# Kernel tuning notes

Measured on AMD Instinct MI355X. Metric: run time of the kernel, lower is better.

Reference implementation:

```python
import jax, jax.numpy as jnp
import numpy as np

HIDDEN = 4096
N_HEADS = 32
N_KV_HEADS = 8
HEAD_DIM = 128
N_GROUPS = N_HEADS // N_KV_HEADS
ROPE_THETA = 10000.0
QMAX = 127.0
B, S = 1, 2048


def setup_inputs() -> dict:
    key = jax.random.key(0)
    ks = jax.random.split(key, 5)
    hidden_states = jax.random.normal(ks[0], (B, S, HIDDEN), dtype=jnp.float32)
    # additive causal mask (Llama style: 0 on/below diagonal, large negative above)
    tril = jnp.tril(jnp.ones((S, S), dtype=bool))
    attention_mask = jnp.where(tril, 0.0, -1e9).astype(jnp.float32)[None, None]
    position_ids = jnp.arange(S, dtype=jnp.int64 if jax.config.jax_enable_x64 else jnp.int32)[None].astype(jnp.int32)
    sc = 1.0 / np.sqrt(HIDDEN)
    wq = jax.random.normal(ks[1], (HIDDEN, N_HEADS * HEAD_DIM), dtype=jnp.float32) * sc
    wk = jax.random.normal(ks[2], (HIDDEN, N_KV_HEADS * HEAD_DIM), dtype=jnp.float32) * sc
    wv = jax.random.normal(ks[3], (HIDDEN, N_KV_HEADS * HEAD_DIM), dtype=jnp.float32) * sc
    wo = jax.random.normal(ks[4], (N_HEADS * HEAD_DIM, HIDDEN), dtype=jnp.float32) * sc
    return {"hidden_states": hidden_states, "attention_mask": attention_mask,
            "position_ids": position_ids, "wq": wq, "wk": wk, "wv": wv, "wo": wo}


def _rope_cos_sin(position_ids):
    # [B, S, HEAD_DIM]
    inv_freq = 1.0 / (ROPE_THETA ** (jnp.arange(0, HEAD_DIM, 2, dtype=jnp.float32) / HEAD_DIM))
    freqs = position_ids.astype(jnp.float32)[..., None] * inv_freq  # [B,S,HEAD_DIM//2]
    emb = jnp.concatenate([freqs, freqs], axis=-1)
    return jnp.cos(emb), jnp.sin(emb)


def _rotate_half(x):
    x1, x2 = jnp.split(x, 2, axis=-1)
    return jnp.concatenate([-x2, x1], axis=-1)


def _fake_quant(x):
    scale = jnp.max(jnp.abs(x)) / QMAX  # global absmax
    return jnp.round(x / scale) * scale


def reference(hidden_states, attention_mask, position_ids, wq, wk, wv, wo):
    bsz, q_len, _ = hidden_states.shape
    q = (hidden_states @ wq).reshape(bsz, q_len, N_HEADS, HEAD_DIM).transpose(0, 2, 1, 3)
    k = (hidden_states @ wk).reshape(bsz, q_len, N_KV_HEADS, HEAD_DIM).transpose(0, 2, 1, 3)
    v = (hidden_states @ wv).reshape(bsz, q_len, N_KV_HEADS, HEAD_DIM).transpose(0, 2, 1, 3)

    cos, sin = _rope_cos_sin(position_ids)  # [B,S,D]
    cos, sin = cos[:, None], sin[:, None]   # broadcast over heads
    q = q * cos + _rotate_half(q) * sin
    k = k * cos + _rotate_half(k) * sin

    # repeat_kv: [B, Hkv, S, D] -> [B, H, S, D]
    k = jnp.repeat(k, N_GROUPS, axis=1)
    v = jnp.repeat(v, N_GROUPS, axis=1)

    # fake quant: global absmax round-trip on Q, K, V
    q = _fake_quant(q)
    k = _fake_quant(k)
    v = _fake_quant(v)

    scores = jnp.einsum('bhqd,bhkd->bhqk', q, k) / np.sqrt(HEAD_DIM)
    scores = scores + attention_mask
    probs = jax.nn.softmax(scores.astype(jnp.float32), axis=-1).astype(q.dtype)
    attn = jnp.einsum('bhqk,bhkd->bhqd', probs, v)
    attn = attn.transpose(0, 2, 1, 3).reshape(bsz, q_len, N_HEADS * HEAD_DIM)
    return attn @ wo
```

## Files before the change

### kernel.cpp

```cpp
#include <hip/hip_runtime.h>
#include <math.h>

#define S_LEN 2048
#define HID 4096
#define NH 32
#define NKV 8
#define HD 128
#define NQKV 6144

typedef __bf16 bf16x8 __attribute__((ext_vector_type(8)));
typedef float f32x4 __attribute__((ext_vector_type(4)));
typedef short short8v __attribute__((ext_vector_type(8)));

__device__ inline short f2bf(float f) {
  union { float f; unsigned u; } a; a.f = f;
  unsigned r = a.u + 0x7fffu + ((a.u >> 16) & 1u);
  return (short)(r >> 16);
}

__device__ inline void glds16(const void* g, void* l) {
  __builtin_amdgcn_global_load_lds((const __attribute__((address_space(1))) void*)g,
                                   (__attribute__((address_space(3))) void*)l, 16, 0, 0);
}

template <int CTRL>
__device__ inline float dpp_max_step(float x) {
  int y = __builtin_amdgcn_update_dpp(0, __float_as_int(x), CTRL, 0xf, 0xf, false);
  return fmaxf(x, __int_as_float(y));
}

__global__ __launch_bounds__(256) void cast_h(const float* __restrict__ X,
                                              short* __restrict__ Y, int n4) {
  int i = blockIdx.x * 256 + threadIdx.x;
  if (i >= n4) return;
  float4 v = ((const float4*)X)[i];
  short4 o;
  o.x = f2bf(v.x); o.y = f2bf(v.y); o.z = f2bf(v.z); o.w = f2bf(v.w);
  ((short4*)Y)[i] = o;
}

__global__ __launch_bounds__(256) void cast_wt(const float* __restrict__ W,
                                               short* __restrict__ Wt, int Ncols) {
  __shared__ float t[32][33];
  int n0 = blockIdx.x * 32, k0 = blockIdx.y * 32;
  int tx = threadIdx.x, ty = threadIdx.y;
  for (int j = 0; j < 4; j++)
    t[ty + 8 * j][tx] = W[(size_t)(k0 + ty + 8 * j) * Ncols + n0 + tx];
  __syncthreads();
  for (int j = 0; j < 4; j++)
    Wt[(size_t)(n0 + ty + 8 * j) * 4096 + k0 + tx] = f2bf(t[tx][ty + 8 * j]);
}

__global__ void rope_table(const int* __restrict__ pos_ids, float* __restrict__ tc,
                           float* __restrict__ ts) {
  int p = blockIdx.x, i = threadIdx.x;
  float pos = (float)pos_ids[p];
  float inv = powf(10000.0f, -((float)(2 * i)) * (1.0f / 128.0f));
  float a = pos * inv;
  tc[p * 64 + i] = cosf(a);
  ts[p * 64 + i] = sinf(a);
}

__global__ __launch_bounds__(256) void rope_absmax(float* __restrict__ C,
                                                   const float* __restrict__ tc,
                                                   const float* __restrict__ ts,
                                                   unsigned* __restrict__ scal) {
  __shared__ float lc[64], lsn[64];
  __shared__ float red[3][4];
  const int p = blockIdx.x, t = threadIdx.x;
  if (t < 64) { lc[t] = tc[p * 64 + t]; lsn[t] = ts[p * 64 + t]; }
  __syncthreads();
  float* row = C + (size_t)p * NQKV;
  float mq = 0.f, mk = 0.f, mv = 0.f;
#pragma unroll
  for (int j = 0; j < 8; j++) {
    int idx = t + 256 * j;
    int i = idx & 63, col = (idx >> 6) * 128 + i;
    float c = lc[i], s = lsn[i];
    float x1 = row[col], x2 = row[col + 64];
    float y1 = x1 * c - x2 * s, y2 = x2 * c + x1 * s;
    row[col] = y1; row[col + 64] = y2;
    mq = fmaxf(mq, fmaxf(fabsf(y1), fabsf(y2)));
  }
#pragma unroll
  for (int j = 0; j < 2; j++) {
    int idx = t + 256 * j;
    int i = idx & 63, col = 4096 + (idx >> 6) * 128 + i;
    float c = lc[i], s = lsn[i];
    float x1 = row[col], x2 = row[col + 64];
    float y1 = x1 * c - x2 * s, y2 = x2 * c + x1 * s;
    row[col] = y1; row[col + 64] = y2;
    mk = fmaxf(mk, fmaxf(fabsf(y1), fabsf(y2)));
  }
#pragma unroll
  for (int j = 0; j < 4; j++) {
    float v = row[5120 + t + 256 * j];
    mv = fmaxf(mv, fabsf(v));
  }
  for (int off = 32; off; off >>= 1) {
    mq = fmaxf(mq, __shfl_xor(mq, off, 64));
    mk = fmaxf(mk, __shfl_xor(mk, off, 64));
    mv = fmaxf(mv, __shfl_xor(mv, off, 64));
  }
  const int wave = t >> 6;
  if ((t & 63) == 0) { red[0][wave] = mq; red[1][wave] = mk; red[2][wave] = mv; }
  __syncthreads();
  if (t < 3) {
    float m = fmaxf(fmaxf(red[t][0], red[t][1]), fmaxf(red[t][2], red[t][3]));
    atomicMax(scal + t, __float_as_uint(m));
  }
}

__global__ __launch_bounds__(256) void quant_q(const float* __restrict__ C,
                                               const unsigned* __restrict__ scal,
                                               short* __restrict__ Qi) {
  int idx = blockIdx.x * 256 + threadIdx.x;
  float scale = __uint_as_float(scal[0]) * (1.0f / 127.0f);
  int p = idx >> 12, c = idx & 4095;
  Qi[idx] = f2bf(rintf(C[(size_t)p * NQKV + c] / scale));
}

__global__ __launch_bounds__(256) void quant_k(const float* __restrict__ C,
                                               const unsigned* __restrict__ scal,
                                               short* __restrict__ Ki) {
  int idx = blockIdx.x * 256 + threadIdx.x;
  float scale = __uint_as_float(scal[1]) * (1.0f / 127.0f);
  int h = idx >> 18, p = (idx >> 7) & 2047, d = idx & 127;
  Ki[idx] = f2bf(rintf(C[(size_t)p * NQKV + 4096 + h * 128 + d] / scale));
}

__global__ __launch_bounds__(256) void quant_vt(const float* __restrict__ C,
                                                const unsigned* __restrict__ scal,
                                                short* __restrict__ Vt) {
  __shared__ float t[64][65];
  int h = blockIdx.x, pt = blockIdx.y, dt = blockIdx.z;
  float scale = __uint_as_float(scal[2]) * (1.0f / 127.0f);
  int tid = threadIdx.x;
  for (int j = 0; j < 16; j++) {
    int q = tid + 256 * j;
    int pl = q >> 6, dl = q & 63;
    t[dl][pl] = C[(size_t)(pt * 64 + pl) * NQKV + 5120 + h * 128 + dt * 64 + dl];
  }
  __syncthreads();
  for (int j = 0; j < 16; j++) {
    int q = tid + 256 * j;
    int dl = q >> 6, pl = q & 63;
    Vt[(size_t)(h * 128 + dt * 64 + dl) * 2048 + pt * 64 + pl] =
        f2bf(rintf(t[dl][pl] / scale));
  }
}

__global__ __launch_bounds__(256, 2) void gemm_bt(const short* __restrict__ A, int lda,
                                                  const short* __restrict__ B,
                                                  float* __restrict__ C, int ldc, int K) {
  __shared__ alignas(16) short As[2][4096];
  __shared__ alignas(16) short Bs[2][4096];
  const int tid = threadIdx.x;
  const int wave = tid >> 6, lane = tid & 63;
  const int quad = lane >> 4, l15 = lane & 15;
  const int m0 = blockIdx.y * 128, n0 = blockIdx.x * 128;
  const int wm = (wave >> 1) * 64, wn = (wave & 1) * 64;
  f32x4 acc[4][4] = {};
  const int sr = wave * 16 + (lane >> 2);
  const int sg = (lane & 3) * 8;
  const short* Ag0 = A + (size_t)(m0 + sr) * lda + sg;
  const short* Ag1 = A + (size_t)(m0 + 64 + sr) * lda + sg;
  const short* Bg0 = B + (size_t)(n0 + sr) * K + sg;
  const short* Bg1 = B + (size_t)(n0 + 64 + sr) * K + sg;
  auto stage = [&](int kk, int b) {
    glds16(Ag0 + kk, &As[b][wave * 512]);
    glds16(Ag1 + kk, &As[b][2048 + wave * 512]);
    glds16(Bg0 + kk, &Bs[b][wave * 512]);
    glds16(Bg1 + kk, &Bs[b][2048 + wave * 512]);
  };
  stage(0, 0);
  int b = 0;
  for (int k0 = 0; k0 < K; k0 += 32) {
    __syncthreads();
    const int nk = (k0 + 32 < K) ? k0 + 32 : k0;
    stage(nk, b ^ 1);
    bf16x8 af[4], bfr[4];
#pragma unroll
    for (int t = 0; t < 4; t++) {
      af[t] = *(const bf16x8*)&As[b][(wm + t * 16 + l15) * 32 + quad * 8];
      bfr[t] = *(const bf16x8*)&Bs[b][(wn + t * 16 + l15) * 32 + quad * 8];
    }
#pragma unroll
    for (int tm = 0; tm < 4; tm++)
#pragma unroll
      for (int tn = 0; tn < 4; tn++)
        acc[tm][tn] =
            __builtin_amdgcn_mfma_f32_16x16x32_bf16(af[tm], bfr[tn], acc[tm][tn], 0, 0, 0);
    b ^= 1;
  }
#pragma unroll
  for (int tm = 0; tm < 4; tm++)
#pragma unroll
    for (int tn = 0; tn < 4; tn++) {
      const int row = m0 + wm + tm * 16 + quad * 4;
      const int col = n0 + wn + tn * 16 + l15;
#pragma unroll
      for (int r = 0; r < 4; r++) C[(size_t)(row + r) * ldc + col] = acc[tm][tn][r];
    }
}

__global__ __launch_bounds__(512, 2) void gemm_bt8(const short* __restrict__ A, int lda,
                                                   const short* __restrict__ B, int ldb,
                                                   float* __restrict__ C, int ldc, int K) {
  __shared__ alignas(16) short As[4][8192];
  __shared__ alignas(16) short Bs[4][8192];
  const int tid = threadIdx.x;
  const int wave = tid >> 6, lane = tid & 63;
  const int quad = lane >> 4, l15 = lane & 15;
  const int wm = wave >> 2, wn = wave & 3;
  const int m0 = blockIdx.y * 256, n0 = blockIdx.x * 256;

  size_t aoff[2], boff[2];
#pragma unroll
  for (int j = 0; j < 2; j++) {
    int c = j * 512 + tid;
    int rp = c >> 3, sp = c & 7;
    int s = sp ^ (rp & 7);
    int row = rp * 2 + (s >> 2);
    int kc = s & 3;
    aoff[j] = (size_t)(m0 + row) * lda + kc * 8;
    boff[j] = (size_t)(n0 + row) * ldb + kc * 8;
  }
  int aro[8], bro[4];
#pragma unroll
  for (int m = 0; m < 8; m++) {
    int row = wm * 128 + m * 16 + l15;
    int rp = row >> 1;
    int s = ((row & 1) << 2) | quad;
    aro[m] = (rp * 8 + (s ^ (rp & 7))) * 8;
  }
#pragma unroll
  for (int n = 0; n < 4; n++) {
    int row = wn * 64 + n * 16 + l15;
    int rp = row >> 1;
    int s = ((row & 1) << 2) | quad;
    bro[n] = (rp * 8 + (s ^ (rp & 7))) * 8;
  }

  const int nt = K >> 5;
  f32x4 acc[8][4] = {};

  auto stageQ = [&](int t2, int b2, int cidx) {
    const int kS = (t2 < nt ? t2 : nt - 1) << 5;
    if (cidx < 2)
      glds16(A + aoff[cidx] + kS, &As[b2][(cidx * 512 + wave * 64) * 8]);
    else
      glds16(B + boff[cidx - 2] + kS, &Bs[b2][((cidx - 2) * 512 + wave * 64) * 8]);
  };

#pragma unroll
  for (int c = 0; c < 4; c++) stageQ(0, 0, c);
#pragma unroll
  for (int c = 0; c < 4; c++) stageQ(1, 1, c);
  asm volatile("s_waitcnt vmcnt(4)" ::: "memory");
  __builtin_amdgcn_s_barrier();

  for (int t = 0; t < nt; t++) {
    const int b = t & 3, b2 = (t + 2) & 3;
    const short* Ab = As[b];
    const short* Bb = Bs[b];
    bf16x8 bf[4], a0, a1;
    stageQ(t + 2, b2, 0);
    bf[0] = *(const bf16x8*)&Bb[bro[0]];
    bf[1] = *(const bf16x8*)&Bb[bro[1]];
    bf[2] = *(const bf16x8*)&Bb[bro[2]];
    bf[3] = *(const bf16x8*)&Bb[bro[3]];
    a0 = *(const bf16x8*)&Ab[aro[0]];
    a1 = *(const bf16x8*)&Ab[aro[1]];
    __builtin_amdgcn_s_barrier();
    __builtin_amdgcn_s_setprio(1);
#pragma unroll
    for (int n = 0; n < 4; n++)
      acc[0][n] = __builtin_amdgcn_mfma_f32_16x16x32_bf16(a0, bf[n], acc[0][n], 0, 0, 0);
#pragma unroll
    for (int n = 0; n < 4; n++)
      acc[1][n] = __builtin_amdgcn_mfma_f32_16x16x32_bf16(a1, bf[n], acc[1][n], 0, 0, 0);
    __builtin_amdgcn_s_setprio(0);
    __builtin_amdgcn_s_barrier();
    stageQ(t + 2, b2, 1);
    a0 = *(const bf16x8*)&Ab[aro[2]];
    a1 = *(const bf16x8*)&Ab[aro[3]];
    __builtin_amdgcn_s_barrier();
    __builtin_amdgcn_s_setprio(1);
#pragma unroll
    for (int n = 0; n < 4; n++)
      acc[2][n] = __builtin_amdgcn_mfma_f32_16x16x32_bf16(a0, bf[n], acc[2][n], 0, 0, 0);
#pragma unroll
    for (int n = 0; n < 4; n++)
      acc[3][n] = __builtin_amdgcn_mfma_f32_16x16x32_bf16(a1, bf[n], acc[3][n], 0, 0, 0);
    __builtin_amdgcn_s_setprio(0);
    __builtin_amdgcn_s_barrier();
    stageQ(t + 2, b2, 2);
    a0 = *(const bf16x8*)&Ab[aro[4]];
    a1 = *(const bf16x8*)&Ab[aro[5]];
    __builtin_amdgcn_s_barrier();
    __builtin_amdgcn_s_setprio(1);
#pragma unroll
    for (int n = 0; n < 4; n++)
      acc[4][n] = __builtin_amdgcn_mfma_f32_16x16x32_bf16(a0, bf[n], acc[4][n], 0, 0, 0);
#pragma unroll
    for (int n = 0; n < 4; n++)
      acc[5][n] = __builtin_amdgcn_mfma_f32_16x16x32_bf16(a1, bf[n], acc[5][n], 0, 0, 0);
    __builtin_amdgcn_s_setprio(0);
    __builtin_amdgcn_s_barrier();
    stageQ(t + 2, b2, 3);
    a0 = *(const bf16x8*)&Ab[aro[6]];
    a1 = *(const bf16x8*)&Ab[aro[7]];
    __builtin_amdgcn_s_barrier();
    __builtin_amdgcn_s_setprio(1);
#pragma unroll
    for (int n = 0; n < 4; n++)
      acc[6][n] = __builtin_amdgcn_mfma_f32_16x16x32_bf16(a0, bf[n], acc[6][n], 0, 0, 0);
#pragma unroll
    for (int n = 0; n < 4; n++)
      acc[7][n] = __builtin_amdgcn_mfma_f32_16x16x32_bf16(a1, bf[n], acc[7][n], 0, 0, 0);
    __builtin_amdgcn_s_setprio(0);
    asm volatile("s_waitcnt vmcnt(4)" ::: "memory");
    __builtin_amdgcn_s_barrier();
    __builtin_amdgcn_sched_barrier(0);
  }
#pragma unroll
  for (int m = 0; m < 8; m++)
#pragma unroll
    for (int n = 0; n < 4; n++) {
      const int row = m0 + wm * 128 + m * 16 + quad * 4;
      const int col = n0 + wn * 64 + n * 16 + l15;
#pragma unroll
      for (int r = 0; r < 4; r++) C[(size_t)(row + r) * ldc + col] = acc[m][n][r];
    }
}

__global__ __launch_bounds__(256, 2) void attn_fused(const short* __restrict__ Qi,
                                                     const short* __restrict__ Ki,
                                                     const short* __restrict__ Vt,
                                                     const unsigned* __restrict__ scal,
                                                     short* __restrict__ Oa) {
  __shared__ alignas(16) short Ks[2][64 * 128];
  __shared__ alignas(16) short Vs[2][128 * 64];
  __shared__ alignas(16) short Ps[4][16 * 72];
  const int tid = threadIdx.x;
  const int wave = tid >> 6, lane = tid & 63;
  const int quad = lane >> 4, l15 = lane & 15;
  const int swz = l15 & 7;
  const int h = blockIdx.x & 31, pq = blockIdx.x >> 5;
  const int kvh = h >> 2;
  const float qs = __uint_as_float(scal[0]) * (1.0f / 127.0f);
  const float ksc = __uint_as_float(scal[1]) * (1.0f / 127.0f);
  const float vsc = __uint_as_float(scal[2]) * (1.0f / 127.0f);
  const float sscale = qs * ksc * 0.08838834764831845f * 1.4426950408889634f;
  const short* Kg = Ki + (size_t)kvh * S_LEN * HD;
  const short* Vg = Vt + (size_t)kvh * HD * S_LEN;

  union { short8v s; bf16x8 b; } uone;
  uone.s = short8v{0x3F80, 0x3F80, 0x3F80, 0x3F80, 0x3F80, 0x3F80, 0x3F80, 0x3F80};
  const bf16x8 vone = uone.b;

  int koff[4], voff[4];
#pragma unroll
  for (int j = 0; j < 4; j++) {
    int slot = j * 256 + tid;
    int r = slot >> 4, seg = slot & 15;
    koff[j] = r * 128 + ((seg ^ (r & 7)) * 8);
    int vr = slot >> 3, vseg = slot & 7;
    voff[j] = vr * 2048 + ((vseg ^ (vr & 7)) * 8);
  }
  auto stage = [&](int k0, int b) {
#pragma unroll
    for (int j = 0; j < 4; j++)
      glds16(Kg + (size_t)k0 * HD + koff[j], &Ks[b][(j * 256 + wave * 64) * 8]);
#pragma unroll
    for (int j = 0; j < 4; j++)
      glds16(Vg + (size_t)k0 + voff[j], &Vs[b][(j * 256 + wave * 64) * 8]);
  };

  stage(0, 0);
  int buf = 0;
  for (int ph = 0; ph < 2; ph++) {
    const int qt = ph ? 31 - pq : pq;
    const int rw = qt * 64 + wave * 16;
    bf16x8 aq[4];
#pragma unroll
    for (int kc = 0; kc < 4; kc++)
      aq[kc] = *(const bf16x8*)(Qi + (size_t)(rw + l15) * 4096 + h * 128 + kc * 32 +
                                quad * 8);
    f32x4 o[9] = {};
    float m_[4] = {-INFINITY, -INFINITY, -INFINITY, -INFINITY};
    const int nkt = qt + 1;
    for (int kt = 0; kt < nkt; kt++) {
      const int k0 = kt * 64;
      __syncthreads();
      const int nx = (kt + 1 < nkt) ? k0 + 64 : 0;
      stage(nx, buf ^ 1);

      const short* Kb = Ks[buf];
      const short* Vb = Vs[buf];
      f32x4 sf[4];
      __builtin_amdgcn_s_setprio(1);
#pragma unroll
      for (int tn = 0; tn < 4; tn++) {
        f32x4 s = {0.f, 0.f, 0.f, 0.f};
#pragma unroll
        for (int kc = 0; kc < 4; kc++) {
          bf16x8 bk = *(const bf16x8*)&Kb[(tn * 16 + l15) * 128 + ((kc * 4 + quad) ^ swz) * 8];
          s = __builtin_amdgcn_mfma_f32_16x16x32_bf16(aq[kc], bk, s, 0, 0, 0);
        }
        sf[tn] = s;
      }
      __builtin_amdgcn_s_setprio(0);

      const bool diag = (kt == qt);
#pragma unroll
      for (int r = 0; r < 4; r++) {
        const int grow = rw + quad * 4 + r;
        float mx = -3.0e38f;
        if (diag) {
#pragma unroll
          for (int tn = 0; tn < 4; tn++) {
            float v = sf[tn][r] * sscale;
            if (k0 + tn * 16 + l15 > grow) v = -3.0e38f;
            sf[tn][r] = v;
            mx = fmaxf(mx, v);
          }
        } else {
#pragma unroll
          for (int tn = 0; tn < 4; tn++) {
            float v = sf[tn][r] * sscale;
            sf[tn][r] = v;
            mx = fmaxf(mx, v);
          }
        }
        mx = dpp_max_step<0x121>(mx);
        mx = dpp_max_step<0x122>(mx);
        mx = dpp_max_step<0x124>(mx);
        mx = dpp_max_step<0x128>(mx);
        const float mo = m_[r];
        const float mn = fmaxf(mo, mx);
        m_[r] = mn;
        const float alpha = __builtin_amdgcn_exp2f(mo - mn);
#pragma unroll
        for (int tn = 0; tn < 4; tn++) {
          float p = __builtin_amdgcn_exp2f(sf[tn][r] - mn);
          Ps[wave][(quad * 4 + r) * 72 + tn * 16 + l15] =
              (short)((__float_as_uint(p) + 0x8000u) >> 16);
        }
        if (__ballot(alpha != 1.0f)) {
#pragma unroll
          for (int t = 0; t < 9; t++) o[t][r] *= alpha;
        }
      }
      __builtin_amdgcn_s_setprio(1);
#pragma unroll
      for (int kk = 0; kk < 2; kk++) {
        bf16x8 ap = *(const bf16x8*)&Ps[wave][l15 * 72 + kk * 32 + quad * 8];
#pragma unroll
        for (int tn = 0; tn < 8; tn++) {
          bf16x8 bv = *(const bf16x8*)&Vb[(tn * 16 + l15) * 64 + ((kk * 4 + quad) ^ swz) * 8];
          o[tn] = __builtin_amdgcn_mfma_f32_16x16x32_bf16(ap, bv, o[tn], 0, 0, 0);
        }
        o[8] = __builtin_amdgcn_mfma_f32_16x16x32_bf16(ap, vone, o[8], 0, 0, 0);
      }
      __builtin_amdgcn_s_setprio(0);
      buf ^= 1;
    }
#pragma unroll
    for (int r = 0; r < 4; r++) {
      const int grow = rw + quad * 4 + r;
      const float sc = vsc / o[8][r];
#pragma unroll
      for (int tn = 0; tn < 8; tn++)
        Oa[(size_t)grow * 4096 + h * 128 + tn * 16 + l15] = f2bf(o[tn][r] * sc);
    }
  }
}

extern "C" void kernel_launch(void* const* d_in, const int* in_sizes, int n_in,
                              void* d_out, int out_size, void* d_ws, size_t ws_size,
                              hipStream_t stream) {
  (void)in_sizes; (void)n_in; (void)out_size; (void)ws_size;
  const float* H  = (const float*)d_in[0];
  const int*   pos = (const int*)d_in[2];
  const float* wq = (const float*)d_in[3];
  const float* wk = (const float*)d_in[4];
  const float* wv = (const float*)d_in[5];
  const float* wo = (const float*)d_in[6];
  char* ws = (char*)d_ws;
  short* Hb   = (short*)(ws + 0);
  short* Wt   = (short*)(ws + 16777216);
  short* Wot  = (short*)(ws + 67108864);
  float* C    = (float*)(ws + 100663296);
  short* Qi   = (short*)(ws + 150994944);
  short* Ki   = (short*)(ws + 167772160);
  short* Vt   = (short*)(ws + 171966464);
  short* Oa   = (short*)(ws + 176160768);
  float* tc   = (float*)(ws + 192937984);
  float* tsn  = (float*)(ws + 193462272);
  unsigned* scal = (unsigned*)(ws + 193986560);

  hipLaunchKernelGGL(cast_h, dim3(8192), dim3(256), 0, stream, H, Hb, 2097152);
  hipLaunchKernelGGL(cast_wt, dim3(128, 128), dim3(32, 8), 0, stream, wq, Wt, 4096);
  hipLaunchKernelGGL(cast_wt, dim3(32, 128), dim3(32, 8), 0, stream, wk,
                     Wt + (size_t)4096 * 4096, 1024);
  hipLaunchKernelGGL(cast_wt, dim3(32, 128), dim3(32, 8), 0, stream, wv,
                     Wt + (size_t)5120 * 4096, 1024);
  hipLaunchKernelGGL(cast_wt, dim3(128, 128), dim3(32, 8), 0, stream, wo, Wot, 4096);
  hipLaunchKernelGGL(rope_table, dim3(2048), dim3(64), 0, stream, pos, tc, tsn);
  hipMemsetAsync(scal, 0, 16, stream);
  hipLaunchKernelGGL(gemm_bt8, dim3(24, 8), dim3(512), 0, stream, Hb, 4096, Wt, 4096, C,
                     6144, 4096);
  hipLaunchKernelGGL(rope_absmax, dim3(2048), dim3(256), 0, stream, C, tc, tsn, scal);
  hipLaunchKernelGGL(quant_q, dim3(32768), dim3(256), 0, stream, C, scal, Qi);
  hipLaunchKernelGGL(quant_k, dim3(8192), dim3(256), 0, stream, C, scal, Ki);
  hipLaunchKernelGGL(quant_vt, dim3(8, 32, 2), dim3(256), 0, stream, C, scal, Vt);
  hipLaunchKernelGGL(attn_fused, dim3(512), dim3(256), 0, stream, Qi, Ki, Vt, scal, Oa);
  hipLaunchKernelGGL(gemm_bt, dim3(32, 16), dim3(256), 0, stream, Oa, 4096, Wot,
                     (float*)d_out, 4096, 4096);
}
```

Measured before the change: 646.4 us.

## Restructure 256x256 GEMM to BK=64 double-buffer with finer staged prefetch

Rewrites the gemm_bt8 main loop to use a K-tile of 64 with two LDS buffers instead of K=32 with a four-deep ring. Global-to-LDS loads for the next tile are split across four phases of the compute loop, each followed by barriers with partial vmcnt waits. The LDS swizzle changes to a row-by-64 XOR layout. The goal is to halve loop iterations and barrier overhead per K and give more MFMA work per sync. The risk is a shallower prefetch depth, which can expose memory latency.

Result: faster. 586.5 us (-9.3%).

```diff
diff --git a/kernel.cpp b/kernel.cpp
--- a/kernel.cpp
+++ b/kernel.cpp
@@ -207,122 +207,85 @@
 __global__ __launch_bounds__(512, 2) void gemm_bt8(const short* __restrict__ A, int lda,
                                                    const short* __restrict__ B, int ldb,
                                                    float* __restrict__ C, int ldc, int K) {
-  __shared__ alignas(16) short As[4][8192];
-  __shared__ alignas(16) short Bs[4][8192];
+  __shared__ alignas(16) short As[2][16384];
+  __shared__ alignas(16) short Bs[2][16384];
   const int tid = threadIdx.x;
   const int wave = tid >> 6, lane = tid & 63;
   const int quad = lane >> 4, l15 = lane & 15;
   const int wm = wave >> 2, wn = wave & 3;
   const int m0 = blockIdx.y * 256, n0 = blockIdx.x * 256;
 
-  size_t aoff[2], boff[2];
-#pragma unroll
-  for (int j = 0; j < 2; j++) {
-    int c = j * 512 + tid;
-    int rp = c >> 3, sp = c & 7;
-    int s = sp ^ (rp & 7);
-    int row = rp * 2 + (s >> 2);
-    int kc = s & 3;
-    aoff[j] = (size_t)(m0 + row) * lda + kc * 8;
-    boff[j] = (size_t)(n0 + row) * ldb + kc * 8;
-  }
-  int aro[8], bro[4];
-#pragma unroll
-  for (int m = 0; m < 8; m++) {
-    int row = wm * 128 + m * 16 + l15;
-    int rp = row >> 1;
-    int s = ((row & 1) << 2) | quad;
-    aro[m] = (rp * 8 + (s ^ (rp & 7))) * 8;
-  }
-#pragma unroll
-  for (int n = 0; n < 4; n++) {
-    int row = wn * 64 + n * 16 + l15;
-    int rp = row >> 1;
-    int s = ((row & 1) << 2) | quad;
-    bro[n] = (rp * 8 + (s ^ (rp & 7))) * 8;
-  }
-
-  const int nt = K >> 5;
+  const int rsub = lane >> 3;
+  const int csw = (lane & 7) ^ rsub;
+  size_t asrc[4], bsrc[4];
+#pragma unroll
+  for (int s = 0; s < 4; s++) {
+    int row = s * 64 + wave * 8 + rsub;
+    asrc[s] = (size_t)(m0 + row) * lda + csw * 8;
+    bsrc[s] = (size_t)(n0 + row) * ldb + csw * 8;
+  }
+  const int nt = K >> 6;
+
+  auto stA = [&](int t2, int s) {
+    const int kk = (t2 < nt ? t2 : nt - 1) << 6;
+    glds16(A + asrc[s] + kk, &As[t2 & 1][(s * 64 + wave * 8) * 64]);
+  };
+  auto stB = [&](int t2, int s) {
+    const int kk = (t2 < nt ? t2 : nt - 1) << 6;
+    glds16(B + bsrc[s] + kk, &Bs[t2 & 1][(s * 64 + wave * 8) * 64]);
+  };
+
+  int swq[2];
+#pragma unroll
+  for (int kc = 0; kc < 2; kc++)
+    swq[kc] = l15 * 64 + (((kc * 4 + quad) ^ (l15 & 7)) * 8);
+
   f32x4 acc[8][4] = {};
 
-  auto stageQ = [&](int t2, int b2, int cidx) {
-    const int kS = (t2 < nt ? t2 : nt - 1) << 5;
-    if (cidx < 2)
-      glds16(A + aoff[cidx] + kS, &As[b2][(cidx * 512 + wave * 64) * 8]);
-    else
-      glds16(B + boff[cidx - 2] + kS, &Bs[b2][((cidx - 2) * 512 + wave * 64) * 8]);
-  };
-
-#pragma unroll
-  for (int c = 0; c < 4; c++) stageQ(0, 0, c);
-#pragma unroll
-  for (int c = 0; c < 4; c++) stageQ(1, 1, c);
-  asm volatile("s_waitcnt vmcnt(4)" ::: "memory");
+  stB(0, 0); stB(0, 1); stB(0, 2); stB(0, 3);
+  stA(0, 0); stA(0, 2); stA(0, 1); stA(0, 3);
+  asm volatile("s_waitcnt vmcnt(2)" ::: "memory");
   __builtin_amdgcn_s_barrier();
 
   for (int t = 0; t < nt; t++) {
-    const int b = t & 3, b2 = (t + 2) & 3;
-    const short* Ab = As[b];
-    const short* Bb = Bs[b];
-    bf16x8 bf[4], a0, a1;
-    stageQ(t + 2, b2, 0);
-    bf[0] = *(const bf16x8*)&Bb[bro[0]];
-    bf[1] = *(const bf16x8*)&Bb[bro[1]];
-    bf[2] = *(const bf16x8*)&Bb[bro[2]];
-    bf[3] = *(const bf16x8*)&Bb[bro[3]];
-    a0 = *(const bf16x8*)&Ab[aro[0]];
-    a1 = *(const bf16x8*)&Ab[aro[1]];
-    __builtin_amdgcn_s_barrier();
-    __builtin_amdgcn_s_setprio(1);
-#pragma unroll
-    for (int n = 0; n < 4; n++)
-      acc[0][n] = __builtin_amdgcn_mfma_f32_16x16x32_bf16(a0, bf[n], acc[0][n], 0, 0, 0);
-#pragma unroll
-    for (int n = 0; n < 4; n++)
-      acc[1][n] = __builtin_amdgcn_mfma_f32_16x16x32_bf16(a1, bf[n], acc[1][n], 0, 0, 0);
-    __builtin_amdgcn_s_setprio(0);
-    __builtin_amdgcn_s_barrier();
-    stageQ(t + 2, b2, 1);
-    a0 = *(const bf16x8*)&Ab[aro[2]];
-    a1 = *(const bf16x8*)&Ab[aro[3]];
-    __builtin_amdgcn_s_barrier();
-    __builtin_amdgcn_s_setprio(1);
-#pragma unroll
-    for (int n = 0; n < 4; n++)
-      acc[2][n] = __builtin_amdgcn_mfma_f32_16x16x32_bf16(a0, bf[n], acc[2][n], 0, 0, 0);
-#pragma unroll
-    for (int n = 0; n < 4; n++)
-      acc[3][n] = __builtin_amdgcn_mfma_f32_16x16x32_bf16(a1, bf[n], acc[3][n], 0, 0, 0);
-    __builtin_amdgcn_s_setprio(0);
-    __builtin_amdgcn_s_barrier();
-    stageQ(t + 2, b2, 2);
-    a0 = *(const bf16x8*)&Ab[aro[4]];
-    a1 = *(const bf16x8*)&Ab[aro[5]];
-    __builtin_amdgcn_s_barrier();
-    __builtin_amdgcn_s_setprio(1);
-#pragma unroll
-    for (int n = 0; n < 4; n++)
-      acc[4][n] = __builtin_amdgcn_mfma_f32_16x16x32_bf16(a0, bf[n], acc[4][n], 0, 0, 0);
-#pragma unroll
-    for (int n = 0; n < 4; n++)
-      acc[5][n] = __builtin_amdgcn_mfma_f32_16x16x32_bf16(a1, bf[n], acc[5][n], 0, 0, 0);
-    __builtin_amdgcn_s_setprio(0);
-    __builtin_amdgcn_s_barrier();
-    stageQ(t + 2, b2, 3);
-    a0 = *(const bf16x8*)&Ab[aro[6]];
-    a1 = *(const bf16x8*)&Ab[aro[7]];
-    __builtin_amdgcn_s_barrier();
-    __builtin_amdgcn_s_setprio(1);
-#pragma unroll
-    for (int n = 0; n < 4; n++)
-      acc[6][n] = __builtin_amdgcn_mfma_f32_16x16x32_bf16(a0, bf[n], acc[6][n], 0, 0, 0);
-#pragma unroll
-    for (int n = 0; n < 4; n++)
-      acc[7][n] = __builtin_amdgcn_mfma_f32_16x16x32_bf16(a1, bf[n], acc[7][n], 0, 0, 0);
-    __builtin_amdgcn_s_setprio(0);
-    asm volatile("s_waitcnt vmcnt(4)" ::: "memory");
-    __builtin_amdgcn_s_barrier();
-    __builtin_amdgcn_sched_barrier(0);
+    const short* Ab = As[t & 1];
+    const short* Bb = Bs[t & 1];
+    bf16x8 bfr[4][2];
+#pragma unroll
+    for (int p = 0; p < 4; p++) {
+      if (p == 0) {
+#pragma unroll
+        for (int n = 0; n < 4; n++)
+#pragma unroll
+          for (int kc = 0; kc < 2; kc++)
+            bfr[n][kc] = *(const bf16x8*)&Bb[(wn * 64 + n * 16) * 64 + swq[kc]];
+      }
+      bf16x8 a0k0 = *(const bf16x8*)&Ab[(wm * 128 + (2 * p) * 16) * 64 + swq[0]];
+      bf16x8 a0k1 = *(const bf16x8*)&Ab[(wm * 128 + (2 * p) * 16) * 64 + swq[1]];
+      bf16x8 a1k0 = *(const bf16x8*)&Ab[(wm * 128 + (2 * p + 1) * 16) * 64 + swq[0]];
+      bf16x8 a1k1 = *(const bf16x8*)&Ab[(wm * 128 + (2 * p + 1) * 16) * 64 + swq[1]];
+      if (p == 0) { stB(t + 1, 0); stB(t + 1, 1); }
+      if (p == 1) { stB(t + 1, 2); stB(t + 1, 3); }
+      if (p == 2) { stA(t + 1, 0); stA(t + 1, 2); }
+      if (p == 3) { stA(t + 1, 1); stA(t + 1, 3); }
+      __builtin_amdgcn_s_barrier();
+      __builtin_amdgcn_s_setprio(1);
+#pragma unroll
+      for (int n = 0; n < 4; n++) {
+        acc[2 * p][n] =
+            __builtin_amdgcn_mfma_f32_16x16x32_bf16(a0k0, bfr[n][0], acc[2 * p][n], 0, 0, 0);
+        acc[2 * p][n] =
+            __builtin_amdgcn_mfma_f32_16x16x32_bf16(a0k1, bfr[n][1], acc[2 * p][n], 0, 0, 0);
+        acc[2 * p + 1][n] = __builtin_amdgcn_mfma_f32_16x16x32_bf16(a1k0, bfr[n][0],
+                                                                    acc[2 * p + 1][n], 0, 0, 0);
+        acc[2 * p + 1][n] = __builtin_amdgcn_mfma_f32_16x16x32_bf16(a1k1, bfr[n][1],
+                                                                    acc[2 * p + 1][n], 0, 0, 0);
+      }
+      __builtin_amdgcn_s_setprio(0);
+      if (p == 1) asm volatile("s_waitcnt vmcnt(4)" ::: "memory");
+      if (p == 3) asm volatile("s_waitcnt vmcnt(2)" ::: "memory");
+      __builtin_amdgcn_s_barrier();
+    }
   }
 #pragma unroll
   for (int m = 0; m < 8; m++)
```
